# Kernel optimization log

Measured on AMD Instinct MI355X. Metric: run time of the kernel, lower is better.

Reference implementation:

```python
import jax, jax.numpy as jnp
import numpy as np

IDIM = 128   # idim == odim (fc1 input dim must match shift-slice width idim_q)
HDIM = 1024
CDIM = 256
IGNORE_OUT = 10000.0


def setup_inputs() -> dict:
    key = jax.random.key(0)
    ks = jax.random.split(key, 4)
    B, T = 4, 512
    x = jax.random.normal(ks[0], (B, T, IDIM), dtype=jnp.float32)
    y = jax.random.normal(ks[1], (B, T, IDIM), dtype=jnp.float32)
    # xavier-ish init for the two linears (bias zeroed, as in initialize())
    w1 = jax.random.normal(ks[2], (HDIM, IDIM), dtype=jnp.float32) / np.sqrt(IDIM).astype(np.float32)
    b1 = jnp.zeros((HDIM,), jnp.float32)
    w2 = jax.random.normal(ks[3], (IDIM, HDIM), dtype=jnp.float32) / np.sqrt(HDIM).astype(np.float32)
    b2 = jnpts = jnp.zeros((IDIM,), jnp.float32)
    return {"x": x, "y": y, "w1": w1, "b1": b1, "w2": w2, "b2": b2}


def _shift_stack(key_seq, idim):
    """Vectorized _pad_for_shift: (B,T,idim) -> (B,T,2*idim-1,idim) shifted slices."""
    pad = idim - 1
    kp = jnp.pad(key_seq, ((0, 0), (0, 0), (pad, pad)))  # (B,T,3*idim-2)
    idx = jnp.arange(2 * idim - 1)[:, None] + jnp.arange(idim)[None, :]  # (S, idim)
    return kp[..., idx]  # (B,T,S,idim)


def _forward(x, y, w1, b1, w2, b2):
    idim = IDIM
    n_iter = HDIM // CDIM
    seq_mask = (y == IGNORE_OUT)                      # (B,T,odim)
    denom = jnp.sum(~seq_mask).astype(x.dtype)
    y_res, x_res = y, x
    losses = []
    for i in range(n_iter):
        # --- argaug (scale=False): sliding cosine cross-correlation + argmax ---
        kpt = _shift_stack(x_res, idim)               # (B,T,S,idim), S=2*idim-1
        num = jnp.einsum('btd,btsd->bts', y_res, kpt)
        den = jnp.linalg.norm(y_res, axis=-1)[..., None] * jnp.linalg.norm(kpt, axis=-1)
        sim = jnp.where(den == 0, 0.0, num / jnp.where(den == 0, 1.0, den))  # NaN(0/0) -> 0
        idx = jnp.argmax(sim, axis=-1)                # (B,T), first max like torch.max
        x_aug = jnp.take_along_axis(kpt, idx[..., None, None], axis=2)[..., 0, :]  # (B,T,idim)
        # --- attention (detached) ---
        attn = jax.lax.stop_gradient(jax.nn.softmax(x_aug * y_res, axis=-1))
        x_attn = x_aug * attn
        # --- _reverse_pad_for_shift: un-shift x_attn by 2*idim-2 - idx ---
        pad = idim - 1
        xap = jnp.pad(x_attn, ((0, 0), (0, 0), (pad, pad)))
        ridx = (2 * idim - 2 - idx)[..., None] + jnp.arange(idim)  # (B,T,idim)
        x_ele = jnp.take_along_axis(xap, ridx, axis=-1)
        # --- channel-masked two-layer MLP ---
        h = x_attn @ w1.T + b1                        # (B,T,hdim)
        m = jnp.zeros((HDIM,), x.dtype).at[i * CDIM:(i + 1) * CDIM].set(1.0)
        y_ele = (h * m) @ w2.T + b2                   # (B,T,odim)
        # --- masked MSE (sum of masked squared errors / #unmasked) ---
        sq = jnp.where(seq_mask, 0.0, (y_ele - y_res) ** 2)
        losses.append(jnp.sum(sq) / denom)
        y_res = y_res - y_ele
        x_res = x_res - x_ele
    return jnp.mean(jnp.stack(losses))


def reference(x, y, w1, b1, w2, b2):
    return _forward(x, y, w1, b1, w2, b2)
```

## Files before the change

### kernel.cpp

```cpp
#include <hip/hip_runtime.h>
#include <math.h>

#define NROWS   2048
#define NITER   4
#define IGNORE_OUT 10000.0f


__device__ __forceinline__ float waveSum(float v){
  #pragma unroll
  for (int o = 32; o; o >>= 1) v += __shfl_down(v, o, 64);
  return v;
}

__device__ __forceinline__ float blkSum(float v, float* red){
  v = waveSum(v);
  int lane = threadIdx.x & 63, wid = threadIdx.x >> 6;
  __syncthreads();
  if (lane == 0) red[wid] = v;
  __syncthreads();
  return red[0] + red[1] + red[2] + red[3];
}

__device__ __forceinline__ float blkMax(float v, float* red){
  #pragma unroll
  for (int o = 32; o; o >>= 1) v = fmaxf(v, __shfl_down(v, o, 64));
  int lane = threadIdx.x & 63, wid = threadIdx.x >> 6;
  __syncthreads();
  if (lane == 0) red[wid] = v;
  __syncthreads();
  return fmaxf(fmaxf(red[0], red[1]), fmaxf(red[2], red[3]));
}

__device__ __forceinline__ int blkArgmaxFirst(float v, int idx, float* redv, int* redi){
  #pragma unroll
  for (int o = 32; o; o >>= 1){
    float ov = __shfl_down(v,   o, 64);
    int   oi = __shfl_down(idx, o, 64);
    if (ov > v || (ov == v && oi < idx)) { v = ov; idx = oi; }
  }
  int lane = threadIdx.x & 63, wid = threadIdx.x >> 6;
  __syncthreads();
  if (lane == 0){ redv[wid] = v; redi[wid] = idx; }
  __syncthreads();
  float bv = redv[0]; int bi = redi[0];
  #pragma unroll
  for (int w = 1; w < 4; ++w){
    float ov = redv[w]; int oi = redi[w];
    if (ov > bv || (ov == bv && oi < bi)) { bv = ov; bi = oi; }
  }
  return bi;
}

__global__ void buildM(const float* __restrict__ w1, const float* __restrict__ w2,
                       float* __restrict__ Mt){
  int blk = blockIdx.x;
  int i = blk >> 7, o = blk & 127;
  int d = threadIdx.x;
  const float* w1p = w1 + (i * 256) * 128 + d;
  const float* w2p = w2 + o * 1024 + i * 256;
  float acc = 0.f;
  #pragma unroll 8
  for (int c = 0; c < 256; ++c)
    acc = fmaf(w1p[c * 128], w2p[c], acc);
  Mt[(i * 128 + d) * 128 + o] = acc;
}

__global__ void biasK(const float* __restrict__ b1, const float* __restrict__ b2,
                      const float* __restrict__ w2, float* __restrict__ biasT){
  int i = blockIdx.x;
  int o = threadIdx.x;
  const float* w2p = w2 + o * 1024 + i * 256;
  const float* b1p = b1 + i * 256;
  float a = b2[o];
  #pragma unroll 8
  for (int c = 0; c < 256; ++c) a = fmaf(b1p[c], w2p[c], a);
  biasT[i * 128 + o] = a;
}

__global__ __launch_bounds__(256)
void mainK(const float* __restrict__ x, const float* __restrict__ y,
           const float* __restrict__ Mt, const float* __restrict__ biasT,
           float* __restrict__ acc){
  __shared__ float xr[128];
  __shared__ float yr[128];
  __shared__ float xatt[128];
  __shared__ float part[256];
  __shared__ float redf[4];
  __shared__ int   redi[4];

  const int tid = threadIdx.x;
  const long base = (long)blockIdx.x * 128;

  float lossAcc = 0.f;
  float cnt = 0.f;
  bool  maskv = false;
  if (tid < 128){
    xr[tid] = x[base + tid];
    float yv = y[base + tid];
    yr[tid] = yv;
    maskv = (yv == IGNORE_OUT);
    cnt = maskv ? 0.f : 1.f;
  }
  __syncthreads();

  for (int i = 0; i < NITER; ++i){
    float sy = (tid < 128) ? yr[tid] * yr[tid] : 0.f;
    float ny2 = blkSum(sy, redf);
    float nY = sqrtf(ny2);

    float num = 0.f, nx2 = 0.f;
    {
      int s  = tid;
      int d0 = 127 - s; if (d0 < 0)   d0 = 0;
      int d1 = 254 - s; if (d1 > 127) d1 = 127;
      int jb = s - 127;
      for (int d = d0; d <= d1; ++d){
        float w = xr[jb + d];
        num = fmaf(yr[d], w, num);
        nx2 = fmaf(w, w, nx2);
      }
    }
    float den = nY * sqrtf(nx2);
    float sim = (den == 0.f) ? 0.f : num / den;
    if (tid >= 255) sim = -INFINITY;
    int sstar = blkArgmaxFirst(sim, tid, redf, redi);

    float xa = 0.f, z = -INFINITY;
    if (tid < 128){
      int j = sstar + tid - 127;
      xa = ((unsigned)j < 128u) ? xr[j] : 0.f;
      z  = xa * yr[tid];
    }
    float mz = blkMax(z, redf);
    float e  = (tid < 128) ? expf(z - mz) : 0.f;
    float se = blkSum(e, redf);
    if (tid < 128) xatt[tid] = xa * (e / se);
    __syncthreads();

    if (tid < 128){
      int j2 = tid + 127 - sstar;
      float xe = ((unsigned)j2 < 128u) ? xatt[j2] : 0.f;
      xr[tid] -= xe;
    }

    {
      int o = tid & 127, half = tid >> 7;
      const float* Mi = Mt + i * 16384 + o;
      int dbeg = half * 64;
      float a2 = 0.f;
      #pragma unroll 8
      for (int d = 0; d < 64; ++d)
        a2 = fmaf(Mi[(dbeg + d) * 128], xatt[dbeg + d], a2);
      part[tid] = a2;
    }
    __syncthreads();
    if (tid < 128){
      float ye   = part[tid] + part[tid + 128] + biasT[i * 128 + tid];
      float diff = ye - yr[tid];
      if (!maskv) lossAcc = fmaf(diff, diff, lossAcc);
      yr[tid] = -diff;
    }
    __syncthreads();
  }

  float tot  = blkSum(lossAcc, redf);
  float totc = blkSum(cnt, redf);
  if (tid == 0){
    atomicAdd(&acc[0], tot);
    atomicAdd(&acc[1], totc);
  }
}

__global__ void finalize(const float* __restrict__ acc, float* __restrict__ out){
  if (threadIdx.x == 0 && blockIdx.x == 0)
    out[0] = acc[0] / ((float)NITER * acc[1]);
}

extern "C" void kernel_launch(void* const* d_in, const int* in_sizes, int n_in,
                              void* d_out, int out_size, void* d_ws, size_t ws_size,
                              hipStream_t stream){
  const float* x  = (const float*)d_in[0];
  const float* y  = (const float*)d_in[1];
  const float* w1 = (const float*)d_in[2];
  const float* b1 = (const float*)d_in[3];
  const float* w2 = (const float*)d_in[4];
  const float* b2 = (const float*)d_in[5];
  float* out = (float*)d_out;

  float* accp  = (float*)d_ws;
  float* Mt    = (float*)((char*)d_ws + 256);
  float* biasT = (float*)((char*)d_ws + 256 + 4 * 128 * 128 * sizeof(float));

  hipMemsetAsync(d_ws, 0, 2 * sizeof(float), stream);
  buildM<<<512, 128, 0, stream>>>(w1, w2, Mt);
  biasK<<<4, 128, 0, stream>>>(b1, b2, w2, biasT);
  mainK<<<NROWS, 256, 0, stream>>>(x, y, Mt, biasT, accp);
  finalize<<<1, 64, 0, stream>>>(accp, out);
}
```

Before: 185.9 us.

## Rewrite main kernel as single-wave per row with shuffle reductions and fused prep

New measurement: 178.9 us. 1.04x faster.

```diff
diff --git a/kernel.cpp b/kernel.cpp
--- a/kernel.cpp
+++ b/kernel.cpp
@@ -5,169 +5,181 @@
 #define NITER   4
 #define IGNORE_OUT 10000.0f
 
-
-__device__ __forceinline__ float waveSum(float v){
+__global__ __launch_bounds__(128)
+void prepK(const float* __restrict__ w1, const float* __restrict__ b1,
+           const float* __restrict__ w2, const float* __restrict__ b2,
+           float* __restrict__ Mt2, float* __restrict__ biasT, float* __restrict__ acc){
+  const int blk = blockIdx.x;
+  const int u = threadIdx.x;
+  if (blk < 512){
+    int i = blk >> 7, o = blk & 127;
+    const float* w1p = w1 + (i * 256) * 128 + u;
+    const float* w2p = w2 + o * 1024 + i * 256;
+    float a = 0.f;
+    #pragma unroll 16
+    for (int c = 0; c < 256; ++c) a = fmaf(w1p[c * 128], w2p[c], a);
+    Mt2[(i * 128 + o) * 128 + u] = a;
+  } else if (blk < 516){
+    int i = blk - 512;
+    const float* w2p = w2 + u * 1024 + i * 256;
+    const float* b1p = b1 + i * 256;
+    float a = b2[u];
+    #pragma unroll 8
+    for (int c = 0; c < 256; ++c) a = fmaf(b1p[c], w2p[c], a);
+    biasT[i * 128 + u] = a;
+  } else {
+    if (u < 2) acc[u] = 0.f;
+  }
+}
+
+__global__ __launch_bounds__(64, 2)
+void mainK(const float* __restrict__ x, const float* __restrict__ y,
+           const float* __restrict__ Mt2, const float* __restrict__ biasT,
+           float* __restrict__ acc){
+  __shared__ alignas(16) float xr[128];
+  __shared__ alignas(16) float xatt[128];
+  __shared__ float yd[384];
+
+  const int l = threadIdx.x;
+  const long base = (long)blockIdx.x * 128;
+
+  float xv0 = x[base + l],      xv1 = x[base + 64 + l];
+  float yv0 = y[base + l],      yv1 = y[base + 64 + l];
+  const bool m0 = (yv0 == IGNORE_OUT), m1 = (yv1 == IGNORE_OUT);
+  float cnt = (m0 ? 0.f : 1.f) + (m1 ? 0.f : 1.f);
+  float lossAcc = 0.f;
+
+  xr[l] = xv0; xr[64 + l] = xv1;
+  yd[128 + l] = yv0; yd[192 + l] = yv1;
+  yd[256 + l] = yv0; yd[320 + l] = yv1;
+  __syncthreads();
+
+  for (int i = 0; i < NITER; ++i){
+    float s0 = xv0 * xv0, s1 = xv1 * xv1;
+    #pragma unroll
+    for (int o2 = 1; o2 < 64; o2 <<= 1){
+      float t0 = __shfl_up(s0, o2, 64);
+      float t1 = __shfl_up(s1, o2, 64);
+      if (l >= o2){ s0 += t0; s1 += t1; }
+    }
+    float tot0  = __shfl(s0, 63, 64);
+    float prefA = s0;
+    float prefB = s1 + tot0;
+    float total = __shfl(s1, 63, 64) + tot0;
+
+    float ny = yv0 * yv0 + yv1 * yv1;
+    #pragma unroll
+    for (int o2 = 32; o2; o2 >>= 1) ny += __shfl_xor(ny, o2, 64);
+    float nY = sqrtf(ny);
+
+    const float* ydpA = yd + (255 - l);
+    const float* ydpB = yd + (191 - l);
+    float ntA = 0.f, n1A = 0.f, ntB = 0.f, n1B = 0.f;
+    #pragma unroll 4
+    for (int j4 = 0; j4 < 64; j4 += 4){
+      float4 x4 = *(const float4*)&xr[j4];
+      float xx[4] = {x4.x, x4.y, x4.z, x4.w};
+      #pragma unroll
+      for (int e = 0; e < 4; ++e){
+        int j = j4 + e;
+        float pA = ydpA[j] * xx[e];
+        float pB = ydpB[j] * xx[e];
+        ntA += pA; n1A += (j <= l) ? pA : 0.f;
+        ntB += pB; n1B += pB;
+      }
+    }
+    #pragma unroll 4
+    for (int j4 = 64; j4 < 128; j4 += 4){
+      float4 x4 = *(const float4*)&xr[j4];
+      float xx[4] = {x4.x, x4.y, x4.z, x4.w};
+      #pragma unroll
+      for (int e = 0; e < 4; ++e){
+        int j = j4 + e;
+        float pA = ydpA[j] * xx[e];
+        float pB = ydpB[j] * xx[e];
+        ntA += pA;
+        ntB += pB; n1B += (j - 64 <= l) ? pB : 0.f;
+      }
+    }
+
+    float bv; int bi;
+    {
+      float numA1 = n1A, numA2 = ntA - n1A;
+      float numB1 = n1B, numB2 = ntB - n1B;
+      float dA1 = nY * sqrtf(prefA);
+      float dB1 = nY * sqrtf(prefB);
+      float dA2 = nY * sqrtf(fmaxf(total - prefA, 0.f));
+      float dB2 = nY * sqrtf(fmaxf(total - prefB, 0.f));
+      float sA1 = (dA1 == 0.f) ? 0.f : numA1 / dA1;
+      float sB1 = (dB1 == 0.f) ? 0.f : numB1 / dB1;
+      float sA2 = (dA2 == 0.f) ? 0.f : numA2 / dA2;
+      float sB2 = (dB2 == 0.f) ? 0.f : numB2 / dB2;
+      if (l == 63) sB2 = -INFINITY;
+      bv = sA1; bi = l;
+      if (sB1 > bv){ bv = sB1; bi = l + 64;  }
+      if (sA2 > bv){ bv = sA2; bi = l + 128; }
+      if (sB2 > bv){ bv = sB2; bi = l + 192; }
+    }
+    #pragma unroll
+    for (int o2 = 1; o2 < 64; o2 <<= 1){
+      float ov = __shfl_xor(bv, o2, 64);
+      int   oi = __shfl_xor(bi, o2, 64);
+      if (ov > bv || (ov == bv && oi < bi)){ bv = ov; bi = oi; }
+    }
+    const int sstar = bi;
+
+    int j0 = sstar + l - 127, j1 = j0 + 64;
+    float xa0 = ((unsigned)j0 < 128u) ? xr[j0] : 0.f;
+    float xa1 = ((unsigned)j1 < 128u) ? xr[j1] : 0.f;
+    float z0 = xa0 * yv0, z1 = xa1 * yv1;
+    float mz = fmaxf(z0, z1);
+    #pragma unroll
+    for (int o2 = 32; o2; o2 >>= 1) mz = fmaxf(mz, __shfl_xor(mz, o2, 64));
+    float e0 = expf(z0 - mz), e1 = expf(z1 - mz);
+    float se = e0 + e1;
+    #pragma unroll
+    for (int o2 = 32; o2; o2 >>= 1) se += __shfl_xor(se, o2, 64);
+    float w0 = xa0 * (e0 / se), w1v = xa1 * (e1 / se);
+    xatt[l] = w0; xatt[64 + l] = w1v;
+    __syncthreads();
+
+    int k0 = l + 127 - sstar, k1 = k0 + 64;
+    xv0 -= ((unsigned)k0 < 128u) ? xatt[k0] : 0.f;
+    xv1 -= ((unsigned)k1 < 128u) ? xatt[k1] : 0.f;
+    xr[l] = xv0; xr[64 + l] = xv1;
+
+    const float* MiA = Mt2 + (i * 128 + l) * 128;
+    const float* MiB = MiA + 64 * 128;
+    float aA = 0.f, aB = 0.f;
+    #pragma unroll 4
+    for (int d4 = 0; d4 < 128; d4 += 4){
+      float4 xa4 = *(const float4*)&xatt[d4];
+      float4 A4  = *(const float4*)&MiA[d4];
+      float4 B4  = *(const float4*)&MiB[d4];
+      aA = fmaf(A4.x, xa4.x, aA); aA = fmaf(A4.y, xa4.y, aA);
+      aA = fmaf(A4.z, xa4.z, aA); aA = fmaf(A4.w, xa4.w, aA);
+      aB = fmaf(B4.x, xa4.x, aB); aB = fmaf(B4.y, xa4.y, aB);
+      aB = fmaf(B4.z, xa4.z, aB); aB = fmaf(B4.w, xa4.w, aB);
+    }
+    float ye0 = aA + biasT[i * 128 + l];
+    float ye1 = aB + biasT[i * 128 + 64 + l];
+    float d0 = ye0 - yv0, d1 = ye1 - yv1;
+    if (!m0) lossAcc = fmaf(d0, d0, lossAcc);
+    if (!m1) lossAcc = fmaf(d1, d1, lossAcc);
+    yv0 = -d0; yv1 = -d1;
+    yd[128 + l] = yv0; yd[192 + l] = yv1;
+    yd[256 + l] = yv0; yd[320 + l] = yv1;
+    __syncthreads();
+  }
+
   #pragma unroll
-  for (int o = 32; o; o >>= 1) v += __shfl_down(v, o, 64);
-  return v;
-}
-
-__device__ __forceinline__ float blkSum(float v, float* red){
-  v = waveSum(v);
-  int lane = threadIdx.x & 63, wid = threadIdx.x >> 6;
-  __syncthreads();
-  if (lane == 0) red[wid] = v;
-  __syncthreads();
-  return red[0] + red[1] + red[2] + red[3];
-}
-
-__device__ __forceinline__ float blkMax(float v, float* red){
-  #pragma unroll
-  for (int o = 32; o; o >>= 1) v = fmaxf(v, __shfl_down(v, o, 64));
-  int lane = threadIdx.x & 63, wid = threadIdx.x >> 6;
-  __syncthreads();
-  if (lane == 0) red[wid] = v;
-  __syncthreads();
-  return fmaxf(fmaxf(red[0], red[1]), fmaxf(red[2], red[3]));
-}
-
-__device__ __forceinline__ int blkArgmaxFirst(float v, int idx, float* redv, int* redi){
-  #pragma unroll
-  for (int o = 32; o; o >>= 1){
-    float ov = __shfl_down(v,   o, 64);
-    int   oi = __shfl_down(idx, o, 64);
-    if (ov > v || (ov == v && oi < idx)) { v = ov; idx = oi; }
-  }
-  int lane = threadIdx.x & 63, wid = threadIdx.x >> 6;
-  __syncthreads();
-  if (lane == 0){ redv[wid] = v; redi[wid] = idx; }
-  __syncthreads();
-  float bv = redv[0]; int bi = redi[0];
-  #pragma unroll
-  for (int w = 1; w < 4; ++w){
-    float ov = redv[w]; int oi = redi[w];
-    if (ov > bv || (ov == bv && oi < bi)) { bv = ov; bi = oi; }
-  }
-  return bi;
-}
-
-__global__ void buildM(const float* __restrict__ w1, const float* __restrict__ w2,
-                       float* __restrict__ Mt){
-  int blk = blockIdx.x;
-  int i = blk >> 7, o = blk & 127;
-  int d = threadIdx.x;
-  const float* w1p = w1 + (i * 256) * 128 + d;
-  const float* w2p = w2 + o * 1024 + i * 256;
-  float acc = 0.f;
-  #pragma unroll 8
-  for (int c = 0; c < 256; ++c)
-    acc = fmaf(w1p[c * 128], w2p[c], acc);
-  Mt[(i * 128 + d) * 128 + o] = acc;
-}
-
-__global__ void biasK(const float* __restrict__ b1, const float* __restrict__ b2,
-                      const float* __restrict__ w2, float* __restrict__ biasT){
-  int i = blockIdx.x;
-  int o = threadIdx.x;
-  const float* w2p = w2 + o * 1024 + i * 256;
-  const float* b1p = b1 + i * 256;
-  float a = b2[o];
-  #pragma unroll 8
-  for (int c = 0; c < 256; ++c) a = fmaf(b1p[c], w2p[c], a);
-  biasT[i * 128 + o] = a;
-}
-
-__global__ __launch_bounds__(256)
-void mainK(const float* __restrict__ x, const float* __restrict__ y,
-           const float* __restrict__ Mt, const float* __restrict__ biasT,
-           float* __restrict__ acc){
-  __shared__ float xr[128];
-  __shared__ float yr[128];
-  __shared__ float xatt[128];
-  __shared__ float part[256];
-  __shared__ float redf[4];
-  __shared__ int   redi[4];
-
-  const int tid = threadIdx.x;
-  const long base = (long)blockIdx.x * 128;
-
-  float lossAcc = 0.f;
-  float cnt = 0.f;
-  bool  maskv = false;
-  if (tid < 128){
-    xr[tid] = x[base + tid];
-    float yv = y[base + tid];
-    yr[tid] = yv;
-    maskv = (yv == IGNORE_OUT);
-    cnt = maskv ? 0.f : 1.f;
-  }
-  __syncthreads();
-
-  for (int i = 0; i < NITER; ++i){
-    float sy = (tid < 128) ? yr[tid] * yr[tid] : 0.f;
-    float ny2 = blkSum(sy, redf);
-    float nY = sqrtf(ny2);
-
-    float num = 0.f, nx2 = 0.f;
-    {
-      int s  = tid;
-      int d0 = 127 - s; if (d0 < 0)   d0 = 0;
-      int d1 = 254 - s; if (d1 > 127) d1 = 127;
-      int jb = s - 127;
-      for (int d = d0; d <= d1; ++d){
-        float w = xr[jb + d];
-        num = fmaf(yr[d], w, num);
-        nx2 = fmaf(w, w, nx2);
-      }
-    }
-    float den = nY * sqrtf(nx2);
-    float sim = (den == 0.f) ? 0.f : num / den;
-    if (tid >= 255) sim = -INFINITY;
-    int sstar = blkArgmaxFirst(sim, tid, redf, redi);
-
-    float xa = 0.f, z = -INFINITY;
-    if (tid < 128){
-      int j = sstar + tid - 127;
-      xa = ((unsigned)j < 128u) ? xr[j] : 0.f;
-      z  = xa * yr[tid];
-    }
-    float mz = blkMax(z, redf);
-    float e  = (tid < 128) ? expf(z - mz) : 0.f;
-    float se = blkSum(e, redf);
-    if (tid < 128) xatt[tid] = xa * (e / se);
-    __syncthreads();
-
-    if (tid < 128){
-      int j2 = tid + 127 - sstar;
-      float xe = ((unsigned)j2 < 128u) ? xatt[j2] : 0.f;
-      xr[tid] -= xe;
-    }
-
-    {
-      int o = tid & 127, half = tid >> 7;
-      const float* Mi = Mt + i * 16384 + o;
-      int dbeg = half * 64;
-      float a2 = 0.f;
-      #pragma unroll 8
-      for (int d = 0; d < 64; ++d)
-        a2 = fmaf(Mi[(dbeg + d) * 128], xatt[dbeg + d], a2);
-      part[tid] = a2;
-    }
-    __syncthreads();
-    if (tid < 128){
-      float ye   = part[tid] + part[tid + 128] + biasT[i * 128 + tid];
-      float diff = ye - yr[tid];
-      if (!maskv) lossAcc = fmaf(diff, diff, lossAcc);
-      yr[tid] = -diff;
-    }
-    __syncthreads();
-  }
-
-  float tot  = blkSum(lossAcc, redf);
-  float totc = blkSum(cnt, redf);
-  if (tid == 0){
-    atomicAdd(&acc[0], tot);
-    atomicAdd(&acc[1], totc);
+  for (int o2 = 32; o2; o2 >>= 1){
+    lossAcc += __shfl_xor(lossAcc, o2, 64);
+    cnt     += __shfl_xor(cnt,     o2, 64);
+  }
+  if (l == 0){
+    atomicAdd(&acc[0], lossAcc);
+    atomicAdd(&acc[1], cnt);
   }
 }
 
@@ -188,12 +200,10 @@
   float* out = (float*)d_out;
 
   float* accp  = (float*)d_ws;
-  float* Mt    = (float*)((char*)d_ws + 256);
+  float* Mt2   = (float*)((char*)d_ws + 256);
   float* biasT = (float*)((char*)d_ws + 256 + 4 * 128 * 128 * sizeof(float));
 
-  hipMemsetAsync(d_ws, 0, 2 * sizeof(float), stream);
-  buildM<<<512, 128, 0, stream>>>(w1, w2, Mt);
-  biasK<<<4, 128, 0, stream>>>(b1, b2, w2, biasT);
-  mainK<<<NROWS, 256, 0, stream>>>(x, y, Mt, biasT, accp);
+  prepK<<<517, 128, 0, stream>>>(w1, b1, w2, b2, Mt2, biasT, accp);
+  mainK<<<NROWS, 64, 0, stream>>>(x, y, Mt2, biasT, accp);
   finalize<<<1, 64, 0, stream>>>(accp, out);
 }
```
